# Kernel tuning notes

Hardware: AMD Instinct MI355X
Metric: run time of the kernel (lower is better)

Reference implementation:

```python
import jax, jax.numpy as jnp
import numpy as np

SPARSITY_RATIO = 0.1


def setup_inputs() -> dict:
    key = jax.random.key(0)
    x = jax.random.normal(key, (4, 4096, 2048), dtype=jnp.float32)
    return {"x": x}


def reference(x):
    # x: [batch, seq_len, n_embd]
    B, S, D = x.shape
    k = max(1, int(D * SPARSITY_RATIO))
    # top-k by absolute value along the feature dim
    _, topk_idx = jax.lax.top_k(jnp.abs(x), k)  # [B, S, k]
    # scatter 1.0 at top-k positions (matches torch scatter_ mask construction)
    b = jnp.arange(B)[:, None, None]
    s = jnp.arange(S)[None, :, None]
    mask = jnp.zeros_like(x).at[b, s, topk_idx].set(1.0)
    scale = jnp.asarray(D / k, dtype=x.dtype)
    return x * mask * scale
```

## Files before the change

### kernel.cpp

```cpp
#include <hip/hip_runtime.h>


constexpr int D_DIM = 2048;
constexpr int K_SEL = 204;
constexpr int NT    = 256;
constexpr int RPW   = 4;

typedef float f32x4 __attribute__((ext_vector_type(4)));

__device__ __forceinline__ f32x4 gload16(const f32x4* p) {
    f32x4 r;
    asm volatile("global_load_dwordx4 %0, %1, off" : "=v"(r) : "v"(p) : "memory");
    return r;
}

#define VMWAIT(n)                                                  \
    do {                                                           \
        asm volatile("s_waitcnt vmcnt(" #n ")" ::: "memory");      \
        __builtin_amdgcn_sched_barrier(0);                         \
    } while (0)

__device__ __forceinline__ int dpp_reduce_add(int x) {
    x += __builtin_amdgcn_update_dpp(0, x, 0x111, 0xF, 0xF, true);
    x += __builtin_amdgcn_update_dpp(0, x, 0x112, 0xF, 0xF, true);
    x += __builtin_amdgcn_update_dpp(0, x, 0x114, 0xF, 0xF, true);
    x += __builtin_amdgcn_update_dpp(0, x, 0x118, 0xF, 0xF, true);
    x += __builtin_amdgcn_update_dpp(0, x, 0x142, 0xA, 0xF, false);
    x += __builtin_amdgcn_update_dpp(0, x, 0x143, 0xC, 0xF, false);
    return __builtin_amdgcn_readlane(x, 63);
}

__device__ __forceinline__ int wave_count_ge(const f32x4 (&f)[8], float t) {
    int c0 = 0, c1 = 0, c2 = 0, c3 = 0;
#pragma unroll
    for (int b = 0; b < 8; ++b) {
        c0 += (__builtin_fabsf(f[b].x) >= t) ? 1 : 0;
        c1 += (__builtin_fabsf(f[b].y) >= t) ? 1 : 0;
        c2 += (__builtin_fabsf(f[b].z) >= t) ? 1 : 0;
        c3 += (__builtin_fabsf(f[b].w) >= t) ? 1 : 0;
    }
    return dpp_reduce_add((c0 + c1) + (c2 + c3));
}

__device__ __forceinline__ void process_row(const f32x4 (&f)[8],
                                            float* __restrict__ outr,
                                            const int lane) {
    const float scale = 2048.0f / 204.0f;

    unsigned lo = 0u, hi = 0x80000000u;
    unsigned thr = 0u;
    bool done = false;

    {
        const int c = wave_count_ge(f, 1.6484375f);
        if (c == K_SEL) { thr = 0x3FD30000u; done = true; }
        else if (c > K_SEL) lo = 0x3FD30000u; else hi = 0x3FD30000u;
    }
    if (!done) {
        const unsigned p2 = (lo != 0u) ? 0x3FD60000u
                                       : 0x3FD00000u;
        const int c = wave_count_ge(f, __uint_as_float(p2));
        if (c == K_SEL) { thr = p2; done = true; }
        else if (c > K_SEL) lo = p2; else hi = p2;
    }
    if (!done) {
        unsigned p3 = 0u;
        if (hi == 0x80000000u)      p3 = 0x3FE00000u;
        else if (lo == 0u)          p3 = 0x3FC80000u;
        if (p3 != 0u) {
            const int c = wave_count_ge(f, __uint_as_float(p3));
            if (c == K_SEL) { thr = p3; done = true; }
            else if (c > K_SEL) lo = p3; else hi = p3;
        }
    }
    if (!done && lo == 0u) {
        const int c = wave_count_ge(f, 1.0f);
        if (c == K_SEL) { thr = 0x3F800000u; done = true; }
        else if (c > K_SEL) lo = 0x3F800000u; else hi = 0x3F800000u;
    }

#pragma unroll 1
    while (!done && (hi - lo) > 1u) {
        const unsigned mid = (lo + hi) >> 1;
        const int c = wave_count_ge(f, __uint_as_float(mid));
        if (c == K_SEL) { thr = mid; done = true; }
        else if (c > K_SEL) lo = mid; else hi = mid;
    }

    f32x4* op = reinterpret_cast<f32x4*>(outr);

    if (done) {
        const float tf = __uint_as_float(thr);
#pragma unroll
        for (int b = 0; b < 8; ++b) {
            f32x4 w;
            w.x = (__builtin_fabsf(f[b].x) >= tf) ? f[b].x * scale : 0.0f;
            w.y = (__builtin_fabsf(f[b].y) >= tf) ? f[b].y * scale : 0.0f;
            w.z = (__builtin_fabsf(f[b].z) >= tf) ? f[b].z * scale : 0.0f;
            w.w = (__builtin_fabsf(f[b].w) >= tf) ? f[b].w * scale : 0.0f;
            __builtin_nontemporal_store(w, op + b * 64 + lane);
        }
        return;
    }

    const float Tf = __uint_as_float(lo);
    int ge_pack = 0;
#pragma unroll
    for (int b = 0; b < 8; ++b) {
        ge_pack += (__builtin_fabsf(f[b].x) > Tf) ? 1 : 0;
        ge_pack += (__builtin_fabsf(f[b].y) > Tf) ? 1 : 0;
        ge_pack += (__builtin_fabsf(f[b].z) > Tf) ? 1 : 0;
        ge_pack += (__builtin_fabsf(f[b].w) > Tf) ? 1 : 0;
        ge_pack += (__builtin_fabsf(f[b].x) == Tf) ? (1 << 16) : 0;
        ge_pack += (__builtin_fabsf(f[b].y) == Tf) ? (1 << 16) : 0;
        ge_pack += (__builtin_fabsf(f[b].z) == Tf) ? (1 << 16) : 0;
        ge_pack += (__builtin_fabsf(f[b].w) == Tf) ? (1 << 16) : 0;
    }
    const int tot = dpp_reduce_add(ge_pack);
    const int cnt_gt = tot & 0xFFFF;
    const int neq = tot >> 16;
    const int r = K_SEL - cnt_gt;

    if (neq == r) {
#pragma unroll
        for (int b = 0; b < 8; ++b) {
            f32x4 w;
            w.x = (__builtin_fabsf(f[b].x) >= Tf) ? f[b].x * scale : 0.0f;
            w.y = (__builtin_fabsf(f[b].y) >= Tf) ? f[b].y * scale : 0.0f;
            w.z = (__builtin_fabsf(f[b].z) >= Tf) ? f[b].z * scale : 0.0f;
            w.w = (__builtin_fabsf(f[b].w) >= Tf) ? f[b].w * scale : 0.0f;
            __builtin_nontemporal_store(w, op + b * 64 + lane);
        }
        return;
    }

    const unsigned long long lt = (lane == 0) ? 0ull : (~0ull >> (64 - lane));
    int base = 0;
    for (int b = 0; b < 8; ++b) {
        const float fe[4] = { f[b].x, f[b].y, f[b].z, f[b].w };
        unsigned long long m[4];
#pragma unroll
        for (int e = 0; e < 4; ++e) m[e] = __ballot(__builtin_fabsf(fe[e]) == Tf);
        int cm = 0;
#pragma unroll
        for (int e = 0; e < 4; ++e) cm += __popcll(m[e] & lt);
        f32x4 w;
        float wv[4];
        int partial = 0;
#pragma unroll
        for (int e = 0; e < 4; ++e) {
            const int rank = base + cm + partial;
            const bool eq = (__builtin_fabsf(fe[e]) == Tf);
            const bool sel = (__builtin_fabsf(fe[e]) > Tf) || (eq && rank < r);
            wv[e] = sel ? fe[e] * scale : 0.0f;
            partial += (int)((m[e] >> lane) & 1ull);
        }
        w.x = wv[0]; w.y = wv[1]; w.z = wv[2]; w.w = wv[3];
        __builtin_nontemporal_store(w, op + b * 64 + lane);
#pragma unroll
        for (int e = 0; e < 4; ++e) base += __popcll(m[e]);
    }
}

__global__ __launch_bounds__(NT) void sparse_topk_kernel(const float* __restrict__ x,
                                                         float* __restrict__ out) {
    const int wave = threadIdx.x >> 6;
    const int lane = threadIdx.x & 63;
    const long long gw = (long long)blockIdx.x * 4 + wave;
    const long long r0 = gw * RPW;

    const f32x4* xp = reinterpret_cast<const f32x4*>(x + r0 * D_DIM);
    float* outr = out + r0 * D_DIM;

    f32x4 A[8], B[8];

#pragma unroll
    for (int b = 0; b < 8; ++b) A[b] = gload16(xp + b * 64 + lane);
#pragma unroll
    for (int b = 0; b < 8; ++b) B[b] = gload16(xp + 512 + b * 64 + lane);

    VMWAIT(8);
    process_row(A, outr, lane);
#pragma unroll
    for (int b = 0; b < 8; ++b) A[b] = gload16(xp + 1024 + b * 64 + lane);

    VMWAIT(16);
    process_row(B, outr + D_DIM, lane);
#pragma unroll
    for (int b = 0; b < 8; ++b) B[b] = gload16(xp + 1536 + b * 64 + lane);

    VMWAIT(16);
    process_row(A, outr + 2 * D_DIM, lane);

    VMWAIT(8);
    process_row(B, outr + 3 * D_DIM, lane);
}

extern "C" void kernel_launch(void* const* d_in, const int* in_sizes, int n_in,
                              void* d_out, int out_size, void* d_ws, size_t ws_size,
                              hipStream_t stream) {
    const float* x = (const float*)d_in[0];
    float* out = (float*)d_out;
    const int rows = in_sizes[0] / D_DIM;
    sparse_topk_kernel<<<rows / (4 * RPW), NT, 0, stream>>>(x, out);
}
```

Baseline: 236.1 us.

## Triple-buffer row loads and process eight rows per wave

Each wave now handles eight rows instead of four and keeps three row buffers in flight instead of two, so more global loads are outstanding while a row is being processed. A launch-bounds hint of two blocks per SM is added, and the output pointer is passed to the row routine already in vector form. The deeper prefetch is meant to hide memory latency behind the per-row threshold search. In exchange it uses more registers and halves the number of launched blocks, which lowers how much parallelism the GPU sees. The fixed vmcnt wait counts also depend on how the nontemporal stores are counted.

```diff
diff --git a/kernel.cpp b/kernel.cpp
--- a/kernel.cpp
+++ b/kernel.cpp
@@ -4,7 +4,7 @@
 constexpr int D_DIM = 2048;
 constexpr int K_SEL = 204;
 constexpr int NT    = 256;
-constexpr int RPW   = 4;
+constexpr int RPW   = 8;
 
 typedef float f32x4 __attribute__((ext_vector_type(4)));
 
@@ -42,8 +42,7 @@
     return dpp_reduce_add((c0 + c1) + (c2 + c3));
 }
 
-__device__ __forceinline__ void process_row(const f32x4 (&f)[8],
-                                            float* __restrict__ outr,
+__device__ __forceinline__ void process_row(const f32x4 (&f)[8], f32x4* op,
                                             const int lane) {
     const float scale = 2048.0f / 204.0f;
 
@@ -86,8 +85,6 @@
         if (c == K_SEL) { thr = mid; done = true; }
         else if (c > K_SEL) lo = mid; else hi = mid;
     }
-
-    f32x4* op = reinterpret_cast<f32x4*>(outr);
 
     if (done) {
         const float tf = __uint_as_float(thr);
@@ -162,38 +159,37 @@
     }
 }
 
-__global__ __launch_bounds__(NT) void sparse_topk_kernel(const float* __restrict__ x,
-                                                         float* __restrict__ out) {
+#define LOADBUF(buf, k)                                                   \
+    do {                                                                  \
+        _Pragma("unroll")                                                 \
+        for (int b = 0; b < 8; ++b)                                       \
+            buf[b] = gload16(xw + (k) * 512 + b * 64 + lane);             \
+    } while (0)
+
+__global__ __launch_bounds__(NT, 2) void sparse_topk_kernel(
+        const float* __restrict__ x, float* __restrict__ out) {
     const int wave = threadIdx.x >> 6;
     const int lane = threadIdx.x & 63;
     const long long gw = (long long)blockIdx.x * 4 + wave;
     const long long r0 = gw * RPW;
 
-    const f32x4* xp = reinterpret_cast<const f32x4*>(x + r0 * D_DIM);
-    float* outr = out + r0 * D_DIM;
-
-    f32x4 A[8], B[8];
-
-#pragma unroll
-    for (int b = 0; b < 8; ++b) A[b] = gload16(xp + b * 64 + lane);
-#pragma unroll
-    for (int b = 0; b < 8; ++b) B[b] = gload16(xp + 512 + b * 64 + lane);
-
-    VMWAIT(8);
-    process_row(A, outr, lane);
-#pragma unroll
-    for (int b = 0; b < 8; ++b) A[b] = gload16(xp + 1024 + b * 64 + lane);
-
-    VMWAIT(16);
-    process_row(B, outr + D_DIM, lane);
-#pragma unroll
-    for (int b = 0; b < 8; ++b) B[b] = gload16(xp + 1536 + b * 64 + lane);
-
-    VMWAIT(16);
-    process_row(A, outr + 2 * D_DIM, lane);
-
-    VMWAIT(8);
-    process_row(B, outr + 3 * D_DIM, lane);
+    const f32x4* xw = reinterpret_cast<const f32x4*>(x + r0 * D_DIM);
+    f32x4* ow = reinterpret_cast<f32x4*>(out + r0 * D_DIM);
+
+    f32x4 A[8], B[8], C[8];
+
+    LOADBUF(A, 0);
+    LOADBUF(B, 1);
+    LOADBUF(C, 2);
+
+    VMWAIT(16); process_row(A, ow + 0 * 512, lane); LOADBUF(A, 3);
+    VMWAIT(16); process_row(B, ow + 1 * 512, lane); LOADBUF(B, 4);
+    VMWAIT(16); process_row(C, ow + 2 * 512, lane); LOADBUF(C, 5);
+    VMWAIT(16); process_row(A, ow + 3 * 512, lane); LOADBUF(A, 6);
+    VMWAIT(16); process_row(B, ow + 4 * 512, lane); LOADBUF(B, 7);
+    VMWAIT(16); process_row(C, ow + 5 * 512, lane);
+    VMWAIT(8);  process_row(A, ow + 6 * 512, lane);
+    VMWAIT(0);  process_row(B, ow + 7 * 512, lane);
 }
 
 extern "C" void kernel_launch(void* const* d_in, const int* in_sizes, int n_in,
```

Result: slower. 241.6 us (+2.3%).
